# Kernel optimization log

Hardware: AMD Instinct MI355X
Metric: run time of the kernel (lower is better)

## Reference

```python
import jax, jax.numpy as jnp
import numpy as np

N_NODES = 50000
N_EDGES = 100000
NODE_DIM = 6
EDGE_DIM = 4
H = 64        # hidden_dim
HEADS = 4
T = 3         # n_iterations
RED = 16      # CBAM reduction ratio
Z_VALUES = np.array([7.98, 22.98, 38.98, 53.98, 89.98, 180.48], np.float32)


def _ln(x, g, b, eps=1e-5):
    mu = jnp.mean(x, -1, keepdims=True)
    v = jnp.mean((x - mu) ** 2, -1, keepdims=True)
    return (x - mu) * jax.lax.rsqrt(v + eps) * g + b


def _conv1d(x, w, b, pad):
    y = jax.lax.conv_general_dilated(x, w, (1,), [(pad, pad)],
                                     dimension_numbers=('NCH', 'OIH', 'NCH'))
    return y + b[None, :, None]


def _cbam(x, w1, b1, w2, b2, cw1, cb1, cw2, cb2):
    # channel attention: pool over node dim -> [1, 2H] -> MLP -> sigmoid
    cat = jnp.concatenate([x.max(0, keepdims=True), x.mean(0, keepdims=True)], 1)
    cw = jax.nn.sigmoid(jnp.maximum(cat @ w1 + b1, 0.0) @ w2 + b2)  # [1, H]
    x = x * cw
    # spatial attention: pool over feature dim -> conv1d stack over node axis
    sp = jnp.stack([x.max(-1), x.mean(-1)], 0)[None]                # [1, 2, N]
    s = jnp.maximum(_conv1d(sp, cw1, cb1, 2), 0.0)
    s = jax.nn.sigmoid(_conv1d(s, cw2, cb2, 1))                     # [1, 1, N]
    return x * s[0, 0][:, None]


def _forward(x, edge_attr, z_table, W_node, b_node, W_edge, b_edge,
             cn_w1, cn_b1, cn_w2, cn_b2, cn_cw1, cn_cb1, cn_cw2, cn_cb2,
             ce_w1, ce_b1, ce_w2, ce_b2, ce_cw1, ce_cb1, ce_cw2, ce_cb2,
             ln_comb_g, ln_comb_b, Wq, bq, Wk, bk, Wv, bv, Wskip, bskip,
             ln_tc_g, ln_tc_b, Wpn, bpn, Wpe, bpe, Wg, bg,
             Wc1, bc1, Wc2, bc2, edge_index, z_keys):
    n = x.shape[0]
    # bidirectional edges
    src = jnp.concatenate([edge_index[0], edge_index[1]])
    dst = jnp.concatenate([edge_index[1], edge_index[0]])
    eab = jnp.concatenate([edge_attr, edge_attr], 0)
    rel = x[src, :3] - x[dst, :3]

    # z embedding lookup (non-matching z -> index 0, matching torch default)
    zint = jnp.round(x[:, 2]).astype(jnp.int32)
    zidx = jnp.argmax(zint[:, None] == z_keys[None, :], 1)

    nf = jnp.maximum(x @ W_node + b_node, 0.0) + z_table[zidx]
    nf = _cbam(nf, cn_w1, cn_b1, cn_w2, cn_b2, cn_cw1, cn_cb1, cn_cw2, cn_cb2)
    ef = jnp.maximum(jnp.concatenate([eab, rel], 1) @ W_edge + b_edge, 0.0)
    ef = _cbam(ef, ce_w1, ce_b1, ce_w2, ce_b2, ce_cw1, ce_cb1, ce_cw2, ce_cb2)

    scale = float(1.0 / np.sqrt(H))
    for i in range(T):
        x0, e0 = nf, ef
        agg = jax.ops.segment_sum(ef, dst, num_segments=n)
        comb = _ln(jnp.concatenate([nf, agg - nf], 1), ln_comb_g[i], ln_comb_b[i])
        # TransformerConv (PyG): q at dst, k/v at src, segment softmax over dst
        q = (comb @ Wq[i] + bq[i]).reshape(n, HEADS, H)
        k = (comb @ Wk[i] + bk[i]).reshape(n, HEADS, H)
        v = (comb @ Wv[i] + bv[i]).reshape(n, HEADS, H)
        logits = jnp.sum(q[dst] * k[src], -1) * scale           # [2E, HEADS]
        m = jax.ops.segment_max(logits, dst, num_segments=n)
        p = jnp.exp(logits - m[dst])
        denom = jax.ops.segment_sum(p, dst, num_segments=n)
        alpha = p / denom[dst]
        out = jax.ops.segment_sum(alpha[..., None] * v[src], dst, num_segments=n)
        out = out.reshape(n, HEADS * H) + comb @ Wskip[i] + bskip[i]
        out = _ln(out, ln_tc_g[i], ln_tc_b[i])
        npj = out @ Wpn[i] + bpn[i]
        epj = out[src] @ Wpe[i] + bpe[i]
        g = jax.nn.sigmoid(jnp.concatenate([x0, npj], 1) @ Wg[i] + bg[i])
        nf = x0 * g + npj * (1.0 - g)
        g2 = jax.nn.sigmoid(jnp.concatenate([e0, epj], 1) @ Wg[i] + bg[i])
        ef = e0 * g2 + epj * (1.0 - g2)

    s_idx, e_idx = edge_index[0], edge_index[1]
    clf = jnp.concatenate([nf[s_idx], nf[e_idx]], 1)
    return (jnp.maximum(clf @ Wc1 + bc1, 0.0) @ Wc2 + bc2)[:, 0]


def setup_inputs() -> dict:
    key = jax.random.key(0)
    ks = iter(jax.random.split(key, 80))
    def nrm(shape, s=0.05):
        return jax.random.normal(next(ks), shape, jnp.float32) * s
    x = jax.random.normal(next(ks), (N_NODES, NODE_DIM), jnp.float32)
    zch = jax.random.randint(next(ks), (N_NODES,), 0, len(Z_VALUES))
    x = x.at[:, 2].set(jnp.asarray(Z_VALUES)[zch])
    edge_index = jax.random.randint(next(ks), (2, N_EDGES), 0, N_NODES)
    edge_attr = jax.random.normal(next(ks), (N_EDGES, EDGE_DIM), jnp.float32)
    z_keys = jnp.asarray(np.round(Z_VALUES).astype(np.int32))
    HH, r = HEADS * H, H // RED
    def zeros(*s):
        return jnp.zeros(s, jnp.float32)
    inp = dict(
        x=x, edge_attr=edge_attr, edge_index=edge_index, z_keys=z_keys,
        z_table=nrm((len(Z_VALUES), H)),
        W_node=nrm((NODE_DIM, H)), b_node=zeros(H),
        W_edge=nrm((EDGE_DIM + 3, H)), b_edge=zeros(H),
        cn_w1=nrm((2 * H, r)), cn_b1=zeros(r), cn_w2=nrm((r, H)), cn_b2=zeros(H),
        cn_cw1=nrm((1, 2, 5)), cn_cb1=zeros(1), cn_cw2=nrm((1, 1, 3)), cn_cb2=zeros(1),
        ce_w1=nrm((2 * H, r)), ce_b1=zeros(r), ce_w2=nrm((r, H)), ce_b2=zeros(H),
        ce_cw1=nrm((1, 2, 5)), ce_cb1=zeros(1), ce_cw2=nrm((1, 1, 3)), ce_cb2=zeros(1),
        ln_comb_g=jnp.ones((T, 2 * H), jnp.float32), ln_comb_b=zeros(T, 2 * H),
        Wq=nrm((T, 2 * H, HH)), bq=zeros(T, HH),
        Wk=nrm((T, 2 * H, HH)), bk=zeros(T, HH),
        Wv=nrm((T, 2 * H, HH)), bv=zeros(T, HH),
        Wskip=nrm((T, 2 * H, HH)), bskip=zeros(T, HH),
        ln_tc_g=jnp.ones((T, HH), jnp.float32), ln_tc_b=zeros(T, HH),
        Wpn=nrm((T, HH, H)), bpn=zeros(T, H),
        Wpe=nrm((T, HH, H)), bpe=zeros(T, H),
        Wg=nrm((T, 2 * H, H)), bg=zeros(T, H),
        Wc1=nrm((2 * H, H)), bc1=zeros(H), Wc2=nrm((H, 1)), bc2=zeros(1),
    )
    return inp


def reference(x, edge_attr, edge_index, z_keys, z_table, W_node, b_node, W_edge, b_edge,
              cn_w1, cn_b1, cn_w2, cn_b2, cn_cw1, cn_cb1, cn_cw2, cn_cb2,
              ce_w1, ce_b1, ce_w2, ce_b2, ce_cw1, ce_cb1, ce_cw2, ce_cb2,
              ln_comb_g, ln_comb_b, Wq, bq, Wk, bk, Wv, bv, Wskip, bskip,
              ln_tc_g, ln_tc_b, Wpn, bpn, Wpe, bpe, Wg, bg, Wc1, bc1, Wc2, bc2):
    return _forward(x, edge_attr, z_table, W_node, b_node, W_edge, b_edge,
                    cn_w1, cn_b1, cn_w2, cn_b2, cn_cw1, cn_cb1, cn_cw2, cn_cb2,
                    ce_w1, ce_b1, ce_w2, ce_b2, ce_cw1, ce_cb1, ce_cw2, ce_cb2,
                    ln_comb_g, ln_comb_b, Wq, bq, Wk, bk, Wv, bv, Wskip, bskip,
                    ln_tc_g, ln_tc_b, Wpn, bpn, Wpe, bpe, Wg, bg,
                    Wc1, bc1, Wc2, bc2, edge_index, z_keys)
```

## Files before the change

### kernel.cpp

```cpp
#include <hip/hip_runtime.h>


#define LN_EPS 1e-5f
#define PBLK 512

typedef __attribute__((ext_vector_type(8))) short bf16x8;
typedef __attribute__((ext_vector_type(4))) float f32x4;

static __device__ __forceinline__ float wsum(float v) {
#pragma unroll
  for (int d = 32; d > 0; d >>= 1) v += __shfl_xor(v, d);
  return v;
}
static __device__ __forceinline__ float sigm(float x) { return 1.0f / (1.0f + __expf(-x)); }
static __device__ __forceinline__ unsigned short f2bf(float f) {
  unsigned int u = __float_as_uint(f);
  u += 0x7FFFu + ((u >> 16) & 1u);
  return (unsigned short)(u >> 16);
}
static __device__ __forceinline__ float bf2f(unsigned short b) {
  return __uint_as_float(((unsigned int)b) << 16);
}

__global__ __launch_bounds__(256) void k_zero2(int* __restrict__ a, int* __restrict__ b, int n) {
  int i = blockIdx.x * 256 + threadIdx.x;
  if (i < n) { a[i] = 0; b[i] = 0; }
}

__global__ __launch_bounds__(256) void k_sentinel(float* __restrict__ out, int n) {
  int i = blockIdx.x * 256 + threadIdx.x;
  if (i < n) out[i] = 1.0e6f;
}

__global__ __launch_bounds__(256) void k_hist(const int* __restrict__ ei, int* __restrict__ cnt, int E) {
  int e = blockIdx.x * 256 + threadIdx.x;
  if (e >= 2 * E) return;
  int d = (e < E) ? ei[E + e] : ei[e - E];
  atomicAdd(&cnt[d], 1);
}

__global__ __launch_bounds__(256) void k_scan1(const int* __restrict__ cnt, int* __restrict__ off,
                                               int* __restrict__ bsum, int n) {
  const int t = threadIdx.x;
  const int lane = t & 63, w = t >> 6;
  const int i0 = blockIdx.x * 1024 + t * 4;
  int v0 = (i0 + 0 < n) ? cnt[i0 + 0] : 0;
  int v1 = (i0 + 1 < n) ? cnt[i0 + 1] : 0;
  int v2 = (i0 + 2 < n) ? cnt[i0 + 2] : 0;
  int v3 = (i0 + 3 < n) ? cnt[i0 + 3] : 0;
  int s = v0 + v1 + v2 + v3;
  int sc = s;
#pragma unroll
  for (int d = 1; d < 64; d <<= 1) {
    int tv = __shfl_up(sc, d);
    if (lane >= d) sc += tv;
  }
  __shared__ int wsums[4];
  if (lane == 63) wsums[w] = sc;
  __syncthreads();
  int wbase = 0;
#pragma unroll
  for (int k = 0; k < 4; ++k)
    if (k < w) wbase += wsums[k];
  int run = wbase + sc - s;
  if (i0 + 0 < n) off[i0 + 0] = run; run += v0;
  if (i0 + 1 < n) off[i0 + 1] = run; run += v1;
  if (i0 + 2 < n) off[i0 + 2] = run; run += v2;
  if (i0 + 3 < n) off[i0 + 3] = run;
  if (t == 255) bsum[blockIdx.x] = wbase + sc;
}

__global__ __launch_bounds__(64) void k_scan2(const int* __restrict__ bsum, int* __restrict__ boff,
                                              int* __restrict__ off, int n, int nblk) {
  const int lane = threadIdx.x;
  int carry = 0;
  for (int base = 0; base < nblk; base += 64) {
    int i = base + lane;
    int v = (i < nblk) ? bsum[i] : 0;
    int sc = v;
#pragma unroll
    for (int d = 1; d < 64; d <<= 1) {
      int tv = __shfl_up(sc, d);
      if (lane >= d) sc += tv;
    }
    if (i < nblk) boff[i] = carry + sc - v;
    carry += __shfl(sc, 63);
  }
  if (lane == 0) off[n] = carry;
}

__global__ __launch_bounds__(256) void k_scan3(int* __restrict__ off, const int* __restrict__ boff, int n) {
  int i = blockIdx.x * 256 + threadIdx.x;
  if (i < n) off[i] += boff[i >> 10];
}

__global__ __launch_bounds__(256) void k_scatter(const int* __restrict__ ei, const int* __restrict__ off,
                                                 int* __restrict__ cur, int* __restrict__ elist,
                                                 int* __restrict__ slist, int E) {
  int e = blockIdx.x * 256 + threadIdx.x;
  if (e >= 2 * E) return;
  int d = (e < E) ? ei[E + e] : ei[e - E];
  int pos = atomicAdd(&cur[d], 1);
  int base = off[d] + pos;
  elist[base] = e;
  slist[base] = ei[e];
}

__global__ __launch_bounds__(256) void k_packW(
    const float* __restrict__ Wq, const float* __restrict__ Wk, const float* __restrict__ Wv,
    const float* __restrict__ Ws, const float* __restrict__ bq, const float* __restrict__ bk,
    const float* __restrict__ bv, const float* __restrict__ bs,
    const float* __restrict__ Wpn, const float* __restrict__ Wpe,
    const float* __restrict__ bpn, const float* __restrict__ bpe,
    const float* __restrict__ Wg, const float* __restrict__ Wc1,
    unsigned short* __restrict__ W1t, float* __restrict__ bias1,
    unsigned short* __restrict__ B2t, float* __restrict__ bias2,
    unsigned short* __restrict__ Wg1t, unsigned short* __restrict__ Wc1t) {
  const int S1 = 3 * 1024 * 128, S2 = 3 * 1024, S3 = 3 * 256 * 256, S4 = 3 * 256;
  const int S5 = 3 * 64 * 64, S6 = 2 * 64 * 64;
  int idx = blockIdx.x * 256 + threadIdx.x;
  if (idx < S1) {
    int i = idx / 131072, r = idx % 131072;
    int col = r >> 7, k = r & 127;
    int m = col >> 8, cc = col & 255;
    const float* W = (m == 0) ? Wq : (m == 1) ? Wk : (m == 2) ? Wv : Ws;
    W1t[idx] = f2bf(W[i * 32768 + k * 256 + cc]);
  } else if (idx < S1 + S2) {
    int j = idx - S1;
    int i = j >> 10, col = j & 1023;
    int m = col >> 8, cc = col & 255;
    const float* bsrc = (m == 0) ? bq : (m == 1) ? bk : (m == 2) ? bv : bs;
    bias1[j] = bsrc[i * 256 + cc];
  } else if (idx < S1 + S2 + S3) {
    int j = idx - S1 - S2;
    int i = j / 65536, r = j % 65536;
    int col = r >> 8, k = r & 255;
    float v;
    if (col < 64) v = Wpn[i * 16384 + k * 64 + col];
    else if (col < 128) v = Wpe[i * 16384 + k * 64 + (col - 64)];
    else {
      const float* Wsrc = (col < 192) ? Wpn : Wpe;
      int cc = col & 63;
      float acc = 0.f;
      for (int jj = 0; jj < 64; ++jj)
        acc = fmaf(Wsrc[i * 16384 + k * 64 + jj], Wg[i * 8192 + (64 + jj) * 64 + cc], acc);
      v = acc;
    }
    B2t[j] = f2bf(v);
  } else if (idx < S1 + S2 + S3 + S4) {
    int j = idx - S1 - S2 - S3;
    int i = j >> 8, col = j & 255;
    float v;
    if (col < 64) v = bpn[i * 64 + col];
    else if (col < 128) v = bpe[i * 64 + col - 64];
    else {
      const float* bsrc = (col < 192) ? bpn : bpe;
      int cc = col & 63;
      float acc = 0.f;
      for (int jj = 0; jj < 64; ++jj)
        acc = fmaf(bsrc[i * 64 + jj], Wg[i * 8192 + (64 + jj) * 64 + cc], acc);
      v = acc;
    }
    bias2[j] = v;
  } else if (idx < S1 + S2 + S3 + S4 + S5) {
    int j = idx - S1 - S2 - S3 - S4;
    int i = j / 4096, r = j % 4096;
    int col = r >> 6, k = r & 63;
    Wg1t[j] = f2bf(Wg[i * 8192 + k * 64 + col]);
  } else if (idx < S1 + S2 + S3 + S4 + S5 + S6) {
    int j = idx - S1 - S2 - S3 - S4 - S5;
    int h = j / 4096, r = j % 4096;
    int col = r >> 6, k = r & 63;
    Wc1t[j] = f2bf(Wc1[(h * 64 + k) * 64 + col]);
  }
}

__global__ __launch_bounds__(256) void k_node_embed(
    const float* __restrict__ x, const int* __restrict__ zk, const float* __restrict__ zt,
    const float* __restrict__ Wn, const float* __restrict__ bn, float* __restrict__ nf, int N) {
  int n = blockIdx.x * 4 + (threadIdx.x >> 6);
  int lane = threadIdx.x & 63;
  if (n >= N) return;
  const float* xr = x + (size_t)n * 6;
  float acc = bn[lane];
#pragma unroll
  for (int d = 0; d < 6; ++d) acc = fmaf(xr[d], Wn[d * 64 + lane], acc);
  int zi = __float2int_rn(xr[2]);
  int idx = 0;
#pragma unroll
  for (int t = 5; t >= 0; --t)
    if (zi == zk[t]) idx = t;
  nf[(size_t)n * 64 + lane] = fmaxf(acc, 0.0f) + zt[idx * 64 + lane];
}

__global__ __launch_bounds__(256) void k_edge_embed(
    const float* __restrict__ x, const float* __restrict__ ea, const int* __restrict__ ei,
    const float* __restrict__ We, const float* __restrict__ be, float* __restrict__ ef, int E) {
  int e = blockIdx.x * 4 + (threadIdx.x >> 6);
  int lane = threadIdx.x & 63;
  if (e >= 2 * E) return;
  int e0 = (e < E) ? e : e - E;
  int s = ei[e];
  int d = (e < E) ? ei[E + e] : ei[e - E];
  const float* ar = ea + (size_t)e0 * 4;
  const float* xs = x + (size_t)s * 6;
  const float* xd = x + (size_t)d * 6;
  float in[7];
  in[0] = ar[0]; in[1] = ar[1]; in[2] = ar[2]; in[3] = ar[3];
  in[4] = xs[0] - xd[0]; in[5] = xs[1] - xd[1]; in[6] = xs[2] - xd[2];
  float acc = be[lane];
#pragma unroll
  for (int dd = 0; dd < 7; ++dd) acc = fmaf(in[dd], We[dd * 64 + lane], acc);
  ef[(size_t)e * 64 + lane] = fmaxf(acc, 0.0f);
}

__global__ __launch_bounds__(256) void k_pool_partial(const float* __restrict__ buf, int n,
                                                      float* __restrict__ pm, float* __restrict__ ps) {
  const int w = threadIdx.x >> 6, l = threadIdx.x & 63;
  const int rsub = l >> 4, c4 = (l & 15) << 2;
  float4 mx = make_float4(-INFINITY, -INFINITY, -INFINITY, -INFINITY);
  float4 sm = make_float4(0.f, 0.f, 0.f, 0.f);
  for (int r = blockIdx.x * 16 + w * 4 + rsub; r < n; r += gridDim.x * 16) {
    float4 v = *(const float4*)(buf + (size_t)r * 64 + c4);
    mx.x = fmaxf(mx.x, v.x); mx.y = fmaxf(mx.y, v.y);
    mx.z = fmaxf(mx.z, v.z); mx.w = fmaxf(mx.w, v.w);
    sm.x += v.x; sm.y += v.y; sm.z += v.z; sm.w += v.w;
  }
#pragma unroll
  for (int d = 16; d < 64; d <<= 1) {
    mx.x = fmaxf(mx.x, __shfl_xor(mx.x, d)); mx.y = fmaxf(mx.y, __shfl_xor(mx.y, d));
    mx.z = fmaxf(mx.z, __shfl_xor(mx.z, d)); mx.w = fmaxf(mx.w, __shfl_xor(mx.w, d));
    sm.x += __shfl_xor(sm.x, d); sm.y += __shfl_xor(sm.y, d);
    sm.z += __shfl_xor(sm.z, d); sm.w += __shfl_xor(sm.w, d);
  }
  __shared__ float smx[4][64], ssm[4][64];
  if (l < 16) {
    *(float4*)&smx[w][c4] = mx;
    *(float4*)&ssm[w][c4] = sm;
  }
  __syncthreads();
  if (threadIdx.x < 64) {
    int t = threadIdx.x;
    float m2 = fmaxf(fmaxf(smx[0][t], smx[1][t]), fmaxf(smx[2][t], smx[3][t]));
    float s2 = ssm[0][t] + ssm[1][t] + ssm[2][t] + ssm[3][t];
    pm[blockIdx.x * 64 + t] = m2;
    ps[blockIdx.x * 64 + t] = s2;
  }
}

__global__ __launch_bounds__(256) void k_pool_final(
    const float* __restrict__ pm, const float* __restrict__ ps, int n, int nblk,
    const float* __restrict__ w1, const float* __restrict__ b1,
    const float* __restrict__ w2, const float* __restrict__ b2, float* __restrict__ cw) {
  __shared__ float redm[4][64], reds[4][64];
  __shared__ float cat[128];
  __shared__ float hid[4];
  int t = threadIdx.x;
  int g = t >> 6, col = t & 63;
  float mx = -INFINITY, sm = 0.0f;
  for (int p = g; p < nblk; p += 4) {
    mx = fmaxf(mx, pm[p * 64 + col]);
    sm += ps[p * 64 + col];
  }
  redm[g][col] = mx;
  reds[g][col] = sm;
  __syncthreads();
  if (t < 64) {
    float m2 = fmaxf(fmaxf(redm[0][t], redm[1][t]), fmaxf(redm[2][t], redm[3][t]));
    float s2 = reds[0][t] + reds[1][t] + reds[2][t] + reds[3][t];
    cat[t] = m2;
    cat[64 + t] = s2 / (float)n;
  }
  __syncthreads();
  if (t < 4) {
    float a = b1[t];
    for (int k = 0; k < 128; ++k) a = fmaf(cat[k], w1[k * 4 + t], a);
    hid[t] = fmaxf(a, 0.0f);
  }
  __syncthreads();
  if (t < 64) {
    float a = b2[t];
#pragma unroll
    for (int h = 0; h < 4; ++h) a = fmaf(hid[h], w2[h * 64 + t], a);
    cw[t] = sigm(a);
  }
}

__global__ __launch_bounds__(256) void k_chan_sp(float* __restrict__ buf, int n,
                                                 const float* __restrict__ cw,
                                                 float* __restrict__ spmax, float* __restrict__ spmean) {
  const int w = threadIdx.x >> 6, l = threadIdx.x & 63;
  const int rsub = l >> 4, c4 = (l & 15) << 2;
  int r = blockIdx.x * 16 + w * 4 + rsub;
  if (r >= n) return;
  float4 cwv = *(const float4*)(cw + c4);
  float4 v = *(const float4*)(buf + (size_t)r * 64 + c4);
  v.x *= cwv.x; v.y *= cwv.y; v.z *= cwv.z; v.w *= cwv.w;
  *(float4*)(buf + (size_t)r * 64 + c4) = v;
  float mx = fmaxf(fmaxf(v.x, v.y), fmaxf(v.z, v.w));
  float sm = v.x + v.y + v.z + v.w;
#pragma unroll
  for (int d = 1; d < 16; d <<= 1) {
    mx = fmaxf(mx, __shfl_xor(mx, d));
    sm += __shfl_xor(sm, d);
  }
  if ((l & 15) == 0) {
    spmax[r] = mx;
    spmean[r] = sm * (1.0f / 64.0f);
  }
}

__global__ __launch_bounds__(256) void k_conv(const float* __restrict__ spmax, const float* __restrict__ spmean,
                                              int n, const float* __restrict__ w1, const float* __restrict__ b1,
                                              const float* __restrict__ w2, const float* __restrict__ b2,
                                              float* __restrict__ s) {
  __shared__ float tl[258];
  int base = blockIdx.x * 256;
  for (int q = threadIdx.x; q < 258; q += 256) {
    int p = base - 1 + q;
    float t = 0.0f;
    if (p >= 0 && p < n) {
      float a = b1[0];
#pragma unroll
      for (int h = 0; h < 5; ++h) {
        int pp = p + h - 2;
        if (pp >= 0 && pp < n) a += spmax[pp] * w1[h] + spmean[pp] * w1[5 + h];
      }
      t = fmaxf(a, 0.0f);
    }
    tl[q] = t;
  }
  __syncthreads();
  int o = base + threadIdx.x;
  if (o < n) {
    float a = b2[0] + tl[threadIdx.x] * w2[0] + tl[threadIdx.x + 1] * w2[1] + tl[threadIdx.x + 2] * w2[2];
    s[o] = sigm(a);
  }
}

__global__ __launch_bounds__(256) void k_row_scale(float* __restrict__ buf, int n, const float* __restrict__ s) {
  int i4 = blockIdx.x * 256 + threadIdx.x;
  if (i4 >= n * 16) return;
  int r = i4 >> 4;
  float sc = s[r];
  float4 v = *(const float4*)(buf + (size_t)i4 * 4);
  v.x *= sc; v.y *= sc; v.z *= sc; v.w *= sc;
  *(float4*)(buf + (size_t)i4 * 4) = v;
}

__global__ __launch_bounds__(256) void k_aggcomb(const float* __restrict__ ef, const float* __restrict__ nf,
                                                 const int* __restrict__ off, const int* __restrict__ elist,
                                                 unsigned short* __restrict__ comb, const float* __restrict__ g,
                                                 const float* __restrict__ b, int N) {
  int n = blockIdx.x * 4 + (threadIdx.x >> 6);
  int lane = threadIdx.x & 63;
  if (n >= N) return;
  float agg = 0.0f;
  int i0 = off[n], i1 = off[n + 1];
  for (int idx = i0; idx < i1; ++idx) agg += ef[(size_t)elist[idx] * 64 + lane];
  float y0 = nf[(size_t)n * 64 + lane];
  float y1 = agg - y0;
  float s1 = wsum(y0 + y1);
  float s2 = wsum(y0 * y0 + y1 * y1);
  float mu = s1 * (1.0f / 128.0f);
  float var = s2 * (1.0f / 128.0f) - mu * mu;
  float rs = rsqrtf(fmaxf(var, 0.0f) + LN_EPS);
  comb[(size_t)n * 128 + lane] = f2bf((y0 - mu) * rs * g[lane] + b[lane]);
  comb[(size_t)n * 128 + 64 + lane] = f2bf((y1 - mu) * rs * g[64 + lane] + b[64 + lane]);
}

template <int MODE>
__global__ __launch_bounds__(256) void gemm_mfma(
    const unsigned short* __restrict__ A, int M, int K,
    const unsigned short* __restrict__ Bt, const float* __restrict__ bias,
    float* __restrict__ outF, unsigned short* __restrict__ outQ,
    unsigned short* __restrict__ outK, unsigned short* __restrict__ outS) {
  constexpr int SHN = (MODE == 0) ? (128 * 136) : (128 * 64 * 2);
  __shared__ unsigned short shmem[SHN];
  unsigned short* As = shmem;
  unsigned short* Bs = shmem + 128 * 64;
  const int tid = threadIdx.x;
  const int bm = blockIdx.x * 128;
  const int bn = blockIdx.y * 128;
  const int wid = tid >> 6, lane = tid & 63;
  const int wr = (wid >> 1) * 64, wc = (wid & 1) * 64;
  const int lrow = lane & 15, lkb = (lane >> 4) * 8;
  f32x4 acc[4][4];
#pragma unroll
  for (int m = 0; m < 4; ++m)
#pragma unroll
    for (int n = 0; n < 4; ++n) acc[m][n] = (f32x4){0.f, 0.f, 0.f, 0.f};

  for (int k0 = 0; k0 < K; k0 += 64) {
#pragma unroll
    for (int l = 0; l < 4; ++l) {
      int c = tid + l * 256;
      int row = c >> 3, kc = (c & 7) * 8;
      int sw = row * 64 + (kc ^ ((row & 7) << 3));
      int grow = bm + row;
      bf16x8 v = {0, 0, 0, 0, 0, 0, 0, 0};
      if (grow < M) v = *(const bf16x8*)(A + (size_t)grow * K + k0 + kc);
      *(bf16x8*)&As[sw] = v;
      int gcol = bn + row;
      *(bf16x8*)&Bs[sw] = *(const bf16x8*)(Bt + (size_t)gcol * K + k0 + kc);
    }
    __syncthreads();
#pragma unroll
    for (int ks = 0; ks < 2; ++ks) {
      const int ke = ks * 32 + lkb;
      bf16x8 af[4], bfr[4];
#pragma unroll
      for (int m = 0; m < 4; ++m) {
        int row = wr + m * 16 + lrow;
        af[m] = *(const bf16x8*)&As[row * 64 + (ke ^ ((row & 7) << 3))];
      }
#pragma unroll
      for (int n = 0; n < 4; ++n) {
        int col = wc + n * 16 + lrow;
        bfr[n] = *(const bf16x8*)&Bs[col * 64 + (ke ^ ((col & 7) << 3))];
      }
#pragma unroll
      for (int m = 0; m < 4; ++m)
#pragma unroll
        for (int n = 0; n < 4; ++n)
          acc[m][n] = __builtin_amdgcn_mfma_f32_16x16x32_bf16(af[m], bfr[n], acc[m][n], 0, 0, 0);
    }
    __syncthreads();
  }

  const int colw = lane & 15, rq = (lane >> 4) * 4;
  if (MODE == 1) {
#pragma unroll
    for (int m = 0; m < 4; ++m) {
#pragma unroll
      for (int n = 0; n < 4; ++n) {
        int gcol = bn + wc + n * 16 + colw;
        float bv = bias[gcol];
#pragma unroll
        for (int r = 0; r < 4; ++r) {
          int grow = bm + wr + m * 16 + rq + r;
          if (grow >= M) continue;
          outF[(size_t)grow * 256 + gcol] = acc[m][n][r] + bv;
        }
      }
    }
  } else {
    unsigned short* Cs = shmem;
#pragma unroll
    for (int m = 0; m < 4; ++m) {
#pragma unroll
      for (int n = 0; n < 4; ++n) {
        int col = wc + n * 16 + colw;
        float bv = bias[bn + col];
#pragma unroll
        for (int r = 0; r < 4; ++r) {
          int row = wr + m * 16 + rq + r;
          Cs[row * 136 + col] = f2bf(acc[m][n][r] + bv);
        }
      }
    }
    __syncthreads();
    const int proj = bn >> 8;
    const int cbase = bn & 255;
    const int rsub = tid >> 4, c8 = (tid & 15) * 8;
#pragma unroll
    for (int i = 0; i < 8; ++i) {
      int row = i * 16 + rsub;
      int grow = bm + row;
      if (grow >= M) continue;
      uint4 v = *(const uint4*)&Cs[row * 136 + c8];
      int cc = cbase + c8;
      if (proj == 0) *(uint4*)(outQ + (size_t)grow * 256 + cc) = v;
      else if (proj == 1) *(uint4*)(outK + (size_t)grow * 512 + cc) = v;
      else if (proj == 2) *(uint4*)(outK + (size_t)grow * 512 + 256 + cc) = v;
      else *(uint4*)(outS + (size_t)grow * 256 + cc) = v;
    }
  }
}

template <int UPD>
__global__ __launch_bounds__(256) void gemm_gate(
    const float* __restrict__ Af, int M, const unsigned short* __restrict__ Wt,
    const float* __restrict__ P, const float* __restrict__ bgv,
    const int* __restrict__ ei, float* __restrict__ upd) {
  __shared__ unsigned short As[128 * 64];
  __shared__ unsigned short Ws[64 * 64];
  const int tid = threadIdx.x;
  const int bm = blockIdx.x * 128;
#pragma unroll
  for (int l = 0; l < 8; ++l) {
    int u = tid + l * 256;
    int row = u >> 4, k4 = (u & 15) << 2;
    int grow = bm + row;
    float4 v = make_float4(0.f, 0.f, 0.f, 0.f);
    if (grow < M) v = *(const float4*)(Af + (size_t)grow * 64 + k4);
    union { unsigned short h[4]; uint2 q; } pk;
    pk.h[0] = f2bf(v.x); pk.h[1] = f2bf(v.y); pk.h[2] = f2bf(v.z); pk.h[3] = f2bf(v.w);
    *(uint2*)&As[row * 64 + (k4 ^ ((row & 7) << 3))] = pk.q;
  }
#pragma unroll
  for (int l = 0; l < 2; ++l) {
    int u = tid + l * 256;
    int row = u >> 3, kc = (u & 7) * 8;
    *(bf16x8*)&Ws[row * 64 + (kc ^ ((row & 7) << 3))] = *(const bf16x8*)(Wt + row * 64 + kc);
  }
  __syncthreads();
  const int wid = tid >> 6, lane = tid & 63;
  const int wr = wid * 32;
  const int lrow = lane & 15, lkb = (lane >> 4) * 8;
  f32x4 acc[2][4];
#pragma unroll
  for (int m = 0; m < 2; ++m)
#pragma unroll
    for (int n = 0; n < 4; ++n) acc[m][n] = (f32x4){0.f, 0.f, 0.f, 0.f};
#pragma unroll
  for (int ks = 0; ks < 2; ++ks) {
    const int ke = ks * 32 + lkb;
    bf16x8 af[2], wf[4];
#pragma unroll
    for (int m = 0; m < 2; ++m) {
      int row = wr + m * 16 + lrow;
      af[m] = *(const bf16x8*)&As[row * 64 + (ke ^ ((row & 7) << 3))];
    }
#pragma unroll
    for (int n = 0; n < 4; ++n) {
      int col = n * 16 + lrow;
      wf[n] = *(const bf16x8*)&Ws[col * 64 + (ke ^ ((col & 7) << 3))];
    }
#pragma unroll
    for (int m = 0; m < 2; ++m)
#pragma unroll
      for (int n = 0; n < 4; ++n)
        acc[m][n] = __builtin_amdgcn_mfma_f32_16x16x32_bf16(af[m], wf[n], acc[m][n], 0, 0, 0);
  }
  const int colw = lane & 15, rq = (lane >> 4) * 4;
#pragma unroll
  for (int m = 0; m < 2; ++m) {
#pragma unroll
    for (int r = 0; r < 4; ++r) {
      int e = bm + wr + m * 16 + rq + r;
      if (e >= M) continue;
      if (UPD == 0) {
#pragma unroll
        for (int n = 0; n < 4; ++n) upd[(size_t)e * 64 + n * 16 + colw] = acc[m][n][r];
      } else {
        int s = (UPD == 2) ? ei[e] : e;
        const float* Pr = P + (size_t)s * 256;
        const int voff = (UPD == 1) ? 128 : 192;
        const int poff = (UPD == 1) ? 0 : 64;
#pragma unroll
        for (int n = 0; n < 4; ++n) {
          int c = n * 16 + colw;
          float g = sigm(acc[m][n][r] + Pr[voff + c] + bgv[c]);
          size_t oi = (size_t)e * 64 + c;
          upd[oi] = upd[oi] * g + Pr[poff + c] * (1.0f - g);
        }
      }
    }
  }
}

__global__ __launch_bounds__(256) void k_attn(const unsigned short* __restrict__ qo,
                                              const unsigned short* __restrict__ kv,
                                              const unsigned short* __restrict__ skipb, const int* __restrict__ off,
                                              const int* __restrict__ slist,
                                              unsigned short* __restrict__ aob,
                                              const float* __restrict__ g, const float* __restrict__ b, int N) {
  int n = blockIdx.x * 4 + (threadIdx.x >> 6);
  int lane = threadIdx.x & 63;
  if (n >= N) return;
  union { uint2 u; unsigned short h[4]; } qq;
  qq.u = *(const uint2*)(qo + (size_t)n * 256 + 4 * lane);
  float q0 = bf2f(qq.h[0]), q1 = bf2f(qq.h[1]), q2 = bf2f(qq.h[2]), q3 = bf2f(qq.h[3]);
  float m = -INFINITY, lsum = 0.f;
  float a0 = 0.f, a1 = 0.f, a2 = 0.f, a3 = 0.f;
  int i0 = off[n], i1 = off[n + 1];
  for (int idx = i0; idx < i1; ++idx) {
    int s = slist[idx];
    const unsigned short* kb = kv + (size_t)s * 512;
    union { uint2 u; unsigned short h[4]; } kk, vv;
    kk.u = *(const uint2*)(kb + 4 * lane);
    vv.u = *(const uint2*)(kb + 256 + 4 * lane);
    float d = q0 * bf2f(kk.h[0]) + q1 * bf2f(kk.h[1]) + q2 * bf2f(kk.h[2]) + q3 * bf2f(kk.h[3]);
#pragma unroll
    for (int dd = 1; dd < 16; dd <<= 1) d += __shfl_xor(d, dd);
    d *= 0.125f;
    float nm = fmaxf(m, d);
    float sc = __expf(m - nm);
    float p = __expf(d - nm);
    lsum = lsum * sc + p;
    a0 = fmaf(p, bf2f(vv.h[0]), a0 * sc);
    a1 = fmaf(p, bf2f(vv.h[1]), a1 * sc);
    a2 = fmaf(p, bf2f(vv.h[2]), a2 * sc);
    a3 = fmaf(p, bf2f(vv.h[3]), a3 * sc);
    m = nm;
  }
  union { uint2 u; unsigned short h[4]; } sb;
  sb.u = *(const uint2*)(skipb + (size_t)n * 256 + 4 * lane);
  float inv = (lsum > 0.f) ? 1.0f / lsum : 0.f;
  float v0 = bf2f(sb.h[0]) + a0 * inv;
  float v1 = bf2f(sb.h[1]) + a1 * inv;
  float v2 = bf2f(sb.h[2]) + a2 * inv;
  float v3 = bf2f(sb.h[3]) + a3 * inv;
  float s1 = wsum(v0 + v1 + v2 + v3);
  float s2 = wsum(v0 * v0 + v1 * v1 + v2 * v2 + v3 * v3);
  float mu = s1 * (1.0f / 256.0f);
  float var = s2 * (1.0f / 256.0f) - mu * mu;
  float rs = rsqrtf(fmaxf(var, 0.0f) + LN_EPS);
  float4 g4 = *(const float4*)(g + 4 * lane);
  float4 b4 = *(const float4*)(b + 4 * lane);
  union { uint2 u; unsigned short h[4]; } ob;
  ob.h[0] = f2bf((v0 - mu) * rs * g4.x + b4.x);
  ob.h[1] = f2bf((v1 - mu) * rs * g4.y + b4.y);
  ob.h[2] = f2bf((v2 - mu) * rs * g4.z + b4.z);
  ob.h[3] = f2bf((v3 - mu) * rs * g4.w + b4.w);
  *(uint2*)(aob + (size_t)n * 256 + 4 * lane) = ob.u;
}

__global__ __launch_bounds__(256) void k_clf_pair(const float* __restrict__ ABt, const float* __restrict__ ABb,
                                                  const int* __restrict__ ei, const float* __restrict__ bc1,
                                                  const float* __restrict__ Wc2, const float* __restrict__ bc2,
                                                  float* __restrict__ out, int E) {
  int e = blockIdx.x * 4 + (threadIdx.x >> 6);
  int lane = threadIdx.x & 63;
  if (e >= E) return;
  int s = ei[e], t = ei[E + e];
  float h = fmaxf(ABt[(size_t)s * 64 + lane] + ABb[(size_t)t * 64 + lane] + bc1[lane], 0.0f);
  float r = wsum(h * Wc2[lane]);
  if (lane == 0) out[e] = r + bc2[0];
}

extern "C" void kernel_launch(void* const* d_in, const int* in_sizes, int n_in,
                              void* d_out, int out_size, void* d_ws, size_t ws_size,
                              hipStream_t stream) {
  const float* x = (const float*)d_in[0];
  const float* edge_attr = (const float*)d_in[1];
  const int* ei = (const int*)d_in[2];
  const int* zk = (const int*)d_in[3];
  const float* z_table = (const float*)d_in[4];
  const float* W_node = (const float*)d_in[5];
  const float* b_node = (const float*)d_in[6];
  const float* W_edge = (const float*)d_in[7];
  const float* b_edge = (const float*)d_in[8];
  const float* cn_w1 = (const float*)d_in[9];
  const float* cn_b1 = (const float*)d_in[10];
  const float* cn_w2 = (const float*)d_in[11];
  const float* cn_b2 = (const float*)d_in[12];
  const float* cn_cw1 = (const float*)d_in[13];
  const float* cn_cb1 = (const float*)d_in[14];
  const float* cn_cw2 = (const float*)d_in[15];
  const float* cn_cb2 = (const float*)d_in[16];
  const float* ce_w1 = (const float*)d_in[17];
  const float* ce_b1 = (const float*)d_in[18];
  const float* ce_w2 = (const float*)d_in[19];
  const float* ce_b2 = (const float*)d_in[20];
  const float* ce_cw1 = (const float*)d_in[21];
  const float* ce_cb1 = (const float*)d_in[22];
  const float* ce_cw2 = (const float*)d_in[23];
  const float* ce_cb2 = (const float*)d_in[24];
  const float* ln_comb_g = (const float*)d_in[25];
  const float* ln_comb_b = (const float*)d_in[26];
  const float* Wq = (const float*)d_in[27];
  const float* bq = (const float*)d_in[28];
  const float* Wk = (const float*)d_in[29];
  const float* bk = (const float*)d_in[30];
  const float* Wv = (const float*)d_in[31];
  const float* bv = (const float*)d_in[32];
  const float* Wskip = (const float*)d_in[33];
  const float* bskip = (const float*)d_in[34];
  const float* ln_tc_g = (const float*)d_in[35];
  const float* ln_tc_b = (const float*)d_in[36];
  const float* Wpn = (const float*)d_in[37];
  const float* bpn = (const float*)d_in[38];
  const float* Wpe = (const float*)d_in[39];
  const float* bpe = (const float*)d_in[40];
  const float* Wg = (const float*)d_in[41];
  const float* bg = (const float*)d_in[42];
  const float* Wc1 = (const float*)d_in[43];
  const float* bc1 = (const float*)d_in[44];
  const float* Wc2 = (const float*)d_in[45];
  const float* bc2 = (const float*)d_in[46];
  float* out = (float*)d_out;

  const int N = in_sizes[0] / 6;
  const int E = in_sizes[2] / 2;
  const int E2 = 2 * E;

  char* p = (char*)d_ws;
  auto carve = [&](size_t bytes) -> void* {
    void* r = (void*)p;
    p += (bytes + 255) & ~(size_t)255;
    return r;
  };
  unsigned short* qo = (unsigned short*)carve((size_t)N * 256 * 2);
  unsigned short* skipb = (unsigned short*)carve((size_t)N * 256 * 2);
  unsigned short* kvb = (unsigned short*)carve((size_t)N * 512 * 2);
  unsigned short* aob = (unsigned short*)carve((size_t)N * 256 * 2);
  float* ef = (float*)carve((size_t)E2 * 64 * 4);
  float* nf = (float*)carve((size_t)N * 64 * 4);
  unsigned short* comb = (unsigned short*)carve((size_t)N * 128 * 2);
  unsigned short* W1t = (unsigned short*)carve((size_t)3 * 1024 * 128 * 2);
  float* bias1 = (float*)carve((size_t)3 * 1024 * 4);
  unsigned short* B2t = (unsigned short*)carve((size_t)3 * 256 * 256 * 2);
  float* bias2 = (float*)carve((size_t)3 * 256 * 4);
  unsigned short* Wg1t = (unsigned short*)carve((size_t)3 * 64 * 64 * 2);
  unsigned short* Wc1t = (unsigned short*)carve((size_t)2 * 64 * 64 * 2);
  int* cnt = (int*)carve((size_t)N * 4);
  int* cur = (int*)carve((size_t)N * 4);
  int* off = (int*)carve((size_t)(N + 1) * 4);
  int* elist = (int*)carve((size_t)E2 * 4);
  int* slist = (int*)carve((size_t)E2 * 4);
  int* bsum = (int*)carve((size_t)256 * 4);
  int* boff = (int*)carve((size_t)256 * 4);
  float* pm = (float*)carve((size_t)PBLK * 64 * 4);
  float* ps = (float*)carve((size_t)PBLK * 64 * 4);
  float* cwv = (float*)carve(64 * 4);
  float* spmax = (float*)carve((size_t)E2 * 4);
  float* spmean = (float*)carve((size_t)E2 * 4);
  float* sconv = (float*)carve((size_t)E2 * 4);
  size_t need = (size_t)(p - (char*)d_ws);

  float* P = (float*)skipb;
  float* ABt = (float*)aob;
  float* ABb = (float*)aob + (size_t)N * 64;

  auto cdiv = [](int a, int b) { return (a + b - 1) / b; };

  if (ws_size < need) {
    k_sentinel<<<cdiv(E, 256), 256, 0, stream>>>(out, E);
    return;
  }

  k_zero2<<<cdiv(N, 256), 256, 0, stream>>>(cnt, cur, N);
  k_hist<<<cdiv(E2, 256), 256, 0, stream>>>(ei, cnt, E);
  const int nblk = cdiv(N, 1024);
  k_scan1<<<nblk, 256, 0, stream>>>(cnt, off, bsum, N);
  k_scan2<<<1, 64, 0, stream>>>(bsum, boff, off, N, nblk);
  k_scan3<<<cdiv(N, 256), 256, 0, stream>>>(off, boff, N);
  k_scatter<<<cdiv(E2, 256), 256, 0, stream>>>(ei, off, cur, elist, slist, E);

  const int PACK = 3 * 1024 * 128 + 3 * 1024 + 3 * 256 * 256 + 3 * 256 + 3 * 64 * 64 + 2 * 64 * 64;
  k_packW<<<cdiv(PACK, 256), 256, 0, stream>>>(Wq, Wk, Wv, Wskip, bq, bk, bv, bskip,
                                               Wpn, Wpe, bpn, bpe, Wg, Wc1,
                                               W1t, bias1, B2t, bias2, Wg1t, Wc1t);

  k_node_embed<<<cdiv(N, 4), 256, 0, stream>>>(x, zk, z_table, W_node, b_node, nf, N);
  k_edge_embed<<<cdiv(E2, 4), 256, 0, stream>>>(x, edge_attr, ei, W_edge, b_edge, ef, E);

  auto run_cbam = [&](float* buf, int rows, const float* w1, const float* b1, const float* w2,
                      const float* b2, const float* cw1, const float* cb1, const float* cw2,
                      const float* cb2) {
    k_pool_partial<<<PBLK, 256, 0, stream>>>(buf, rows, pm, ps);
    k_pool_final<<<1, 256, 0, stream>>>(pm, ps, rows, PBLK, w1, b1, w2, b2, cwv);
    k_chan_sp<<<cdiv(rows, 16), 256, 0, stream>>>(buf, rows, cwv, spmax, spmean);
    k_conv<<<cdiv(rows, 256), 256, 0, stream>>>(spmax, spmean, rows, cw1, cb1, cw2, cb2, sconv);
    k_row_scale<<<cdiv(rows * 16, 256), 256, 0, stream>>>(buf, rows, sconv);
  };
  run_cbam(nf, N, cn_w1, cn_b1, cn_w2, cn_b2, cn_cw1, cn_cb1, cn_cw2, cn_cb2);
  run_cbam(ef, E2, ce_w1, ce_b1, ce_w2, ce_b2, ce_cw1, ce_cb1, ce_cw2, ce_cb2);

  dim3 gqkvs(cdiv(N, 128), 8);
  dim3 gp(cdiv(N, 128), 2);
  for (int i = 0; i < 3; ++i) {
    k_aggcomb<<<cdiv(N, 4), 256, 0, stream>>>(ef, nf, off, elist, comb,
                                              ln_comb_g + (size_t)i * 128, ln_comb_b + (size_t)i * 128, N);
    gemm_mfma<0><<<gqkvs, 256, 0, stream>>>(comb, N, 128, W1t + (size_t)i * 131072,
                                            bias1 + (size_t)i * 1024, nullptr, qo, kvb, skipb);
    k_attn<<<cdiv(N, 4), 256, 0, stream>>>(qo, kvb, skipb, off, slist, aob,
                                           ln_tc_g + (size_t)i * 256, ln_tc_b + (size_t)i * 256, N);
    gemm_mfma<1><<<gp, 256, 0, stream>>>(aob, N, 256, B2t + (size_t)i * 65536,
                                         bias2 + (size_t)i * 256, P, nullptr, nullptr, nullptr);
    gemm_gate<1><<<cdiv(N, 128), 256, 0, stream>>>(nf, N, Wg1t + (size_t)i * 4096, P,
                                                   bg + (size_t)i * 64, nullptr, nf);
    gemm_gate<2><<<cdiv(E2, 128), 256, 0, stream>>>(ef, E2, Wg1t + (size_t)i * 4096, P,
                                                    bg + (size_t)i * 64, ei, ef);
  }

  gemm_gate<0><<<cdiv(N, 128), 256, 0, stream>>>(nf, N, Wc1t, nullptr, nullptr, nullptr, ABt);
  gemm_gate<0><<<cdiv(N, 128), 256, 0, stream>>>(nf, N, Wc1t + 4096, nullptr, nullptr, nullptr, ABb);
  k_clf_pair<<<cdiv(E, 4), 256, 0, stream>>>(ABt, ABb, ei, bc1, Wc2, bc2, out, E);
  (void)out_size;
  (void)n_in;
}
```

Baseline: 868.7 us.

## Store edge features in bf16 and unroll attention loop by two

The edge feature buffer (200k x 64) changes from fp32 to bf16 storage, and every kernel that reads or writes it (edge embed, CBAM pool/scale, aggregation, edge gate GEMM) gets a templated or bf16 path. This halves edge-feature memory traffic and lets the gate GEMM load bf16 tiles directly, with no conversion step. The attention kernel also processes two neighbours per iteration so more loads are in flight. The cost is extra rounding of edge features on every update across iterations, which may drift from the fp32 reference.

Result: faster. 802.1 us (-7.7%).

```diff
diff --git a/kernel.cpp b/kernel.cpp
--- a/kernel.cpp
+++ b/kernel.cpp
@@ -20,6 +20,18 @@
 }
 static __device__ __forceinline__ float bf2f(unsigned short b) {
   return __uint_as_float(((unsigned int)b) << 16);
+}
+static __device__ __forceinline__ float4 ld4v(const float* p) { return *(const float4*)p; }
+static __device__ __forceinline__ float4 ld4v(const unsigned short* p) {
+  union { uint2 u; unsigned short h[4]; } t;
+  t.u = *(const uint2*)p;
+  return make_float4(bf2f(t.h[0]), bf2f(t.h[1]), bf2f(t.h[2]), bf2f(t.h[3]));
+}
+static __device__ __forceinline__ void st4v(float* p, float4 v) { *(float4*)p = v; }
+static __device__ __forceinline__ void st4v(unsigned short* p, float4 v) {
+  union { uint2 u; unsigned short h[4]; } t;
+  t.h[0] = f2bf(v.x); t.h[1] = f2bf(v.y); t.h[2] = f2bf(v.z); t.h[3] = f2bf(v.w);
+  *(uint2*)p = t.u;
 }
 
 __global__ __launch_bounds__(256) void k_zero2(int* __restrict__ a, int* __restrict__ b, int n) {
@@ -195,7 +207,8 @@
 
 __global__ __launch_bounds__(256) void k_edge_embed(
     const float* __restrict__ x, const float* __restrict__ ea, const int* __restrict__ ei,
-    const float* __restrict__ We, const float* __restrict__ be, float* __restrict__ ef, int E) {
+    const float* __restrict__ We, const float* __restrict__ be,
+    unsigned short* __restrict__ ef, int E) {
   int e = blockIdx.x * 4 + (threadIdx.x >> 6);
   int lane = threadIdx.x & 63;
   if (e >= 2 * E) return;
@@ -211,17 +224,18 @@
   float acc = be[lane];
 #pragma unroll
   for (int dd = 0; dd < 7; ++dd) acc = fmaf(in[dd], We[dd * 64 + lane], acc);
-  ef[(size_t)e * 64 + lane] = fmaxf(acc, 0.0f);
-}
-
-__global__ __launch_bounds__(256) void k_pool_partial(const float* __restrict__ buf, int n,
+  ef[(size_t)e * 64 + lane] = f2bf(fmaxf(acc, 0.0f));
+}
+
+template <typename T>
+__global__ __launch_bounds__(256) void k_pool_partial(const T* __restrict__ buf, int n,
                                                       float* __restrict__ pm, float* __restrict__ ps) {
   const int w = threadIdx.x >> 6, l = threadIdx.x & 63;
   const int rsub = l >> 4, c4 = (l & 15) << 2;
   float4 mx = make_float4(-INFINITY, -INFINITY, -INFINITY, -INFINITY);
   float4 sm = make_float4(0.f, 0.f, 0.f, 0.f);
   for (int r = blockIdx.x * 16 + w * 4 + rsub; r < n; r += gridDim.x * 16) {
-    float4 v = *(const float4*)(buf + (size_t)r * 64 + c4);
+    float4 v = ld4v(buf + (size_t)r * 64 + c4);
     mx.x = fmaxf(mx.x, v.x); mx.y = fmaxf(mx.y, v.y);
     mx.z = fmaxf(mx.z, v.z); mx.w = fmaxf(mx.w, v.w);
     sm.x += v.x; sm.y += v.y; sm.z += v.z; sm.w += v.w;
@@ -286,7 +300,8 @@
   }
 }
 
-__global__ __launch_bounds__(256) void k_chan_sp(float* __restrict__ buf, int n,
+template <typename T>
+__global__ __launch_bounds__(256) void k_chan_sp(T* __restrict__ buf, int n,
                                                  const float* __restrict__ cw,
                                                  float* __restrict__ spmax, float* __restrict__ spmean) {
   const int w = threadIdx.x >> 6, l = threadIdx.x & 63;
@@ -294,9 +309,9 @@
   int r = blockIdx.x * 16 + w * 4 + rsub;
   if (r >= n) return;
   float4 cwv = *(const float4*)(cw + c4);
-  float4 v = *(const float4*)(buf + (size_t)r * 64 + c4);
+  float4 v = ld4v(buf + (size_t)r * 64 + c4);
   v.x *= cwv.x; v.y *= cwv.y; v.z *= cwv.z; v.w *= cwv.w;
-  *(float4*)(buf + (size_t)r * 64 + c4) = v;
+  st4v(buf + (size_t)r * 64 + c4, v);
   float mx = fmaxf(fmaxf(v.x, v.y), fmaxf(v.z, v.w));
   float sm = v.x + v.y + v.z + v.w;
 #pragma unroll
@@ -338,17 +353,19 @@
   }
 }
 
-__global__ __launch_bounds__(256) void k_row_scale(float* __restrict__ buf, int n, const float* __restrict__ s) {
+template <typename T>
+__global__ __launch_bounds__(256) void k_row_scale(T* __restrict__ buf, int n, const float* __restrict__ s) {
   int i4 = blockIdx.x * 256 + threadIdx.x;
   if (i4 >= n * 16) return;
   int r = i4 >> 4;
   float sc = s[r];
-  float4 v = *(const float4*)(buf + (size_t)i4 * 4);
+  float4 v = ld4v(buf + (size_t)i4 * 4);
   v.x *= sc; v.y *= sc; v.z *= sc; v.w *= sc;
-  *(float4*)(buf + (size_t)i4 * 4) = v;
-}
-
-__global__ __launch_bounds__(256) void k_aggcomb(const float* __restrict__ ef, const float* __restrict__ nf,
+  st4v(buf + (size_t)i4 * 4, v);
+}
+
+__global__ __launch_bounds__(256) void k_aggcomb(const unsigned short* __restrict__ ef,
+                                                 const float* __restrict__ nf,
                                                  const int* __restrict__ off, const int* __restrict__ elist,
                                                  unsigned short* __restrict__ comb, const float* __restrict__ g,
                                                  const float* __restrict__ b, int N) {
@@ -357,7 +374,7 @@
   if (n >= N) return;
   float agg = 0.0f;
   int i0 = off[n], i1 = off[n + 1];
-  for (int idx = i0; idx < i1; ++idx) agg += ef[(size_t)elist[idx] * 64 + lane];
+  for (int idx = i0; idx < i1; ++idx) agg += bf2f(ef[(size_t)elist[idx] * 64 + lane]);
   float y0 = nf[(size_t)n * 64 + lane];
   float y1 = agg - y0;
   float s1 = wsum(y0 + y1);
@@ -480,23 +497,37 @@
 
 template <int UPD>
 __global__ __launch_bounds__(256) void gemm_gate(
-    const float* __restrict__ Af, int M, const unsigned short* __restrict__ Wt,
+    const void* __restrict__ Av, int M, const unsigned short* __restrict__ Wt,
     const float* __restrict__ P, const float* __restrict__ bgv,
-    const int* __restrict__ ei, float* __restrict__ upd) {
+    const int* __restrict__ ei, void* __restrict__ updv) {
   __shared__ unsigned short As[128 * 64];
   __shared__ unsigned short Ws[64 * 64];
   const int tid = threadIdx.x;
   const int bm = blockIdx.x * 128;
-#pragma unroll
-  for (int l = 0; l < 8; ++l) {
-    int u = tid + l * 256;
-    int row = u >> 4, k4 = (u & 15) << 2;
-    int grow = bm + row;
-    float4 v = make_float4(0.f, 0.f, 0.f, 0.f);
-    if (grow < M) v = *(const float4*)(Af + (size_t)grow * 64 + k4);
-    union { unsigned short h[4]; uint2 q; } pk;
-    pk.h[0] = f2bf(v.x); pk.h[1] = f2bf(v.y); pk.h[2] = f2bf(v.z); pk.h[3] = f2bf(v.w);
-    *(uint2*)&As[row * 64 + (k4 ^ ((row & 7) << 3))] = pk.q;
+  if (UPD == 2) {
+    const unsigned short* Ab = (const unsigned short*)Av;
+#pragma unroll
+    for (int l = 0; l < 4; ++l) {
+      int u = tid + l * 256;
+      int row = u >> 3, kc = (u & 7) * 8;
+      int grow = bm + row;
+      bf16x8 v = {0, 0, 0, 0, 0, 0, 0, 0};
+      if (grow < M) v = *(const bf16x8*)(Ab + (size_t)grow * 64 + kc);
+      *(bf16x8*)&As[row * 64 + (kc ^ ((row & 7) << 3))] = v;
+    }
+  } else {
+    const float* Af = (const float*)Av;
+#pragma unroll
+    for (int l = 0; l < 8; ++l) {
+      int u = tid + l * 256;
+      int row = u >> 4, k4 = (u & 15) << 2;
+      int grow = bm + row;
+      float4 v = make_float4(0.f, 0.f, 0.f, 0.f);
+      if (grow < M) v = *(const float4*)(Af + (size_t)grow * 64 + k4);
+      union { unsigned short h[4]; uint2 q; } pk;
+      pk.h[0] = f2bf(v.x); pk.h[1] = f2bf(v.y); pk.h[2] = f2bf(v.z); pk.h[3] = f2bf(v.w);
+      *(uint2*)&As[row * 64 + (k4 ^ ((row & 7) << 3))] = pk.q;
+    }
   }
 #pragma unroll
   for (int l = 0; l < 2; ++l) {
@@ -541,19 +572,30 @@
       int e = bm + wr + m * 16 + rq + r;
       if (e >= M) continue;
       if (UPD == 0) {
+        float* upd = (float*)updv;
 #pragma unroll
         for (int n = 0; n < 4; ++n) upd[(size_t)e * 64 + n * 16 + colw] = acc[m][n][r];
-      } else {
-        int s = (UPD == 2) ? ei[e] : e;
-        const float* Pr = P + (size_t)s * 256;
-        const int voff = (UPD == 1) ? 128 : 192;
-        const int poff = (UPD == 1) ? 0 : 64;
+      } else if (UPD == 1) {
+        float* upd = (float*)updv;
+        const float* Pr = P + (size_t)e * 256;
 #pragma unroll
         for (int n = 0; n < 4; ++n) {
           int c = n * 16 + colw;
-          float g = sigm(acc[m][n][r] + Pr[voff + c] + bgv[c]);
+          float g = sigm(acc[m][n][r] + Pr[128 + c] + bgv[c]);
           size_t oi = (size_t)e * 64 + c;
-          upd[oi] = upd[oi] * g + Pr[poff + c] * (1.0f - g);
+          upd[oi] = upd[oi] * g + Pr[c] * (1.0f - g);
+        }
+      } else {
+        unsigned short* upd = (unsigned short*)updv;
+        int s = ei[e];
+        const float* Pr = P + (size_t)s * 256;
+#pragma unroll
+        for (int n = 0; n < 4; ++n) {
+          int c = n * 16 + colw;
+          float g = sigm(acc[m][n][r] + Pr[192 + c] + bgv[c]);
+          size_t oi = (size_t)e * 64 + c;
+          float vA = bf2f(upd[oi]);
+          upd[oi] = f2bf(vA * g + Pr[64 + c] * (1.0f - g));
         }
       }
     }
@@ -575,7 +617,42 @@
   float m = -INFINITY, lsum = 0.f;
   float a0 = 0.f, a1 = 0.f, a2 = 0.f, a3 = 0.f;
   int i0 = off[n], i1 = off[n + 1];
-  for (int idx = i0; idx < i1; ++idx) {
+  int idx = i0;
+  for (; idx + 2 <= i1; idx += 2) {
+    int sA = slist[idx], sB = slist[idx + 1];
+    const unsigned short* kbA = kv + (size_t)sA * 512;
+    const unsigned short* kbB = kv + (size_t)sB * 512;
+    union { uint2 u; unsigned short h[4]; } kkA, vvA, kkB, vvB;
+    kkA.u = *(const uint2*)(kbA + 4 * lane);
+    vvA.u = *(const uint2*)(kbA + 256 + 4 * lane);
+    kkB.u = *(const uint2*)(kbB + 4 * lane);
+    vvB.u = *(const uint2*)(kbB + 256 + 4 * lane);
+    float dA = q0 * bf2f(kkA.h[0]) + q1 * bf2f(kkA.h[1]) + q2 * bf2f(kkA.h[2]) + q3 * bf2f(kkA.h[3]);
+    float dB = q0 * bf2f(kkB.h[0]) + q1 * bf2f(kkB.h[1]) + q2 * bf2f(kkB.h[2]) + q3 * bf2f(kkB.h[3]);
+#pragma unroll
+    for (int dd = 1; dd < 16; dd <<= 1) {
+      dA += __shfl_xor(dA, dd);
+      dB += __shfl_xor(dB, dd);
+    }
+    dA *= 0.125f;
+    dB *= 0.125f;
+    float nm, sc, p;
+    nm = fmaxf(m, dA); sc = __expf(m - nm); p = __expf(dA - nm);
+    lsum = lsum * sc + p;
+    a0 = fmaf(p, bf2f(vvA.h[0]), a0 * sc);
+    a1 = fmaf(p, bf2f(vvA.h[1]), a1 * sc);
+    a2 = fmaf(p, bf2f(vvA.h[2]), a2 * sc);
+    a3 = fmaf(p, bf2f(vvA.h[3]), a3 * sc);
+    m = nm;
+    nm = fmaxf(m, dB); sc = __expf(m - nm); p = __expf(dB - nm);
+    lsum = lsum * sc + p;
+    a0 = fmaf(p, bf2f(vvB.h[0]), a0 * sc);
+    a1 = fmaf(p, bf2f(vvB.h[1]), a1 * sc);
+    a2 = fmaf(p, bf2f(vvB.h[2]), a2 * sc);
+    a3 = fmaf(p, bf2f(vvB.h[3]), a3 * sc);
+    m = nm;
+  }
+  if (idx < i1) {
     int s = slist[idx];
     const unsigned short* kb = kv + (size_t)s * 512;
     union { uint2 u; unsigned short h[4]; } kk, vv;
@@ -696,7 +773,7 @@
   unsigned short* skipb = (unsigned short*)carve((size_t)N * 256 * 2);
   unsigned short* kvb = (unsigned short*)carve((size_t)N * 512 * 2);
   unsigned short* aob = (unsigned short*)carve((size_t)N * 256 * 2);
-  float* ef = (float*)carve((size_t)E2 * 64 * 4);
+  unsigned short* efb = (unsigned short*)carve((size_t)E2 * 64 * 2);
   float* nf = (float*)carve((size_t)N * 64 * 4);
   unsigned short* comb = (unsigned short*)carve((size_t)N * 128 * 2);
   unsigned short* W1t = (unsigned short*)carve((size_t)3 * 1024 * 128 * 2);
@@ -745,24 +822,24 @@
                                                W1t, bias1, B2t, bias2, Wg1t, Wc1t);
 
   k_node_embed<<<cdiv(N, 4), 256, 0, stream>>>(x, zk, z_table, W_node, b_node, nf, N);
-  k_edge_embed<<<cdiv(E2, 4), 256, 0, stream>>>(x, edge_attr, ei, W_edge, b_edge, ef, E);
-
-  auto run_cbam = [&](float* buf, int rows, const float* w1, const float* b1, const float* w2,
-                      const float* b2, const float* cw1, const float* cb1, const float* cw2,
-                      const float* cb2) {
-    k_pool_partial<<<PBLK, 256, 0, stream>>>(buf, rows, pm, ps);
-    k_pool_final<<<1, 256, 0, stream>>>(pm, ps, rows, PBLK, w1, b1, w2, b2, cwv);
-    k_chan_sp<<<cdiv(rows, 16), 256, 0, stream>>>(buf, rows, cwv, spmax, spmean);
-    k_conv<<<cdiv(rows, 256), 256, 0, stream>>>(spmax, spmean, rows, cw1, cb1, cw2, cb2, sconv);
-    k_row_scale<<<cdiv(rows * 16, 256), 256, 0, stream>>>(buf, rows, sconv);
-  };
-  run_cbam(nf, N, cn_w1, cn_b1, cn_w2, cn_b2, cn_cw1, cn_cb1, cn_cw2, cn_cb2);
-  run_cbam(ef, E2, ce_w1, ce_b1, ce_w2, ce_b2, ce_cw1, ce_cb1, ce_cw2, ce_cb2);
+  k_edge_embed<<<cdiv(E2, 4), 256, 0, stream>>>(x, edge_attr, ei, W_edge, b_edge, efb, E);
+
+  k_pool_partial<float><<<PBLK, 256, 0, stream>>>(nf, N, pm, ps);
+  k_pool_final<<<1, 256, 0, stream>>>(pm, ps, N, PBLK, cn_w1, cn_b1, cn_w2, cn_b2, cwv);
+  k_chan_sp<float><<<cdiv(N, 16), 256, 0, stream>>>(nf, N, cwv, spmax, spmean);
+  k_conv<<<cdiv(N, 256), 256, 0, stream>>>(spmax, spmean, N, cn_cw1, cn_cb1, cn_cw2, cn_cb2, sconv);
+  k_row_scale<float><<<cdiv(N * 16, 256), 256, 0, stream>>>(nf, N, sconv);
+
+  k_pool_partial<unsigned short><<<PBLK, 256, 0, stream>>>(efb, E2, pm, ps);
+  k_pool_final<<<1, 256, 0, stream>>>(pm, ps, E2, PBLK, ce_w1, ce_b1, ce_w2, ce_b2, cwv);
+  k_chan_sp<unsigned short><<<cdiv(E2, 16), 256, 0, stream>>>(efb, E2, cwv, spmax, spmean);
+  k_conv<<<cdiv(E2, 256), 256, 0, stream>>>(spmax, spmean, E2, ce_cw1, ce_cb1, ce_cw2, ce_cb2, sconv);
+  k_row_scale<unsigned short><<<cdiv(E2 * 16, 256), 256, 0, stream>>>(efb, E2, sconv);
 
   dim3 gqkvs(cdiv(N, 128), 8);
   dim3 gp(cdiv(N, 128), 2);
   for (int i = 0; i < 3; ++i) {
-    k_aggcomb<<<cdiv(N, 4), 256, 0, stream>>>(ef, nf, off, elist, comb,
+    k_aggcomb<<<cdiv(N, 4), 256, 0, stream>>>(efb, nf, off, elist, comb,
                                               ln_comb_g + (size_t)i * 128, ln_comb_b + (size_t)i * 128, N);
     gemm_mfma<0><<<gqkvs, 256, 0, stream>>>(comb, N, 128, W1t + (size_t)i * 131072,
                                             bias1 + (size_t)i * 1024, nullptr, qo, kvb, skipb);
@@ -772,8 +849,8 @@
                                          bias2 + (size_t)i * 256, P, nullptr, nullptr, nullptr);
     gemm_gate<1><<<cdiv(N, 128), 256, 0, stream>>>(nf, N, Wg1t + (size_t)i * 4096, P,
                                                    bg + (size_t)i * 64, nullptr, nf);
-    gemm_gate<2><<<cdiv(E2, 128), 256, 0, stream>>>(ef, E2, Wg1t + (size_t)i * 4096, P,
-                                                    bg + (size_t)i * 64, ei, ef);
+    gemm_gate<2><<<cdiv(E2, 128), 256, 0, stream>>>(efb, E2, Wg1t + (size_t)i * 4096, P,
+                                                    bg + (size_t)i * 64, ei, efb);
   }
 
   gemm_gate<0><<<cdiv(N, 128), 256, 0, stream>>>(nf, N, Wc1t, nullptr, nullptr, nullptr, ABt);
```
